# Optimization experiments

Hardware: AMD Instinct MI355X
Metric: run time of the kernel (lower is better)

The kernel has to match this reference:

```python
import jax, jax.numpy as jnp
import numpy as np

D = 128           # embed_dim
NUM_LAYERS = 2
N_CLASSES = 4
OUT_CELL = 64
SPEAKERS = 2
INPUT_DIMS = [768, 74, 35]
B, T = 32, 60


def setup_inputs() -> dict:
    key = jax.random.key(0)
    ks = jax.random.split(key, 24)
    inp = {}
    inp['x0'] = jax.random.normal(ks[0], (B, T, INPUT_DIMS[0]), jnp.float32)
    inp['x1'] = jax.random.normal(ks[1], (B, T, INPUT_DIMS[1]), jnp.float32)
    inp['x2'] = jax.random.normal(ks[2], (B, T, INPUT_DIMS[2]), jnp.float32)
    inp['smask'] = jax.random.normal(ks[3], (B, T, SPEAKERS), jnp.float32)  # argmax -> speaker ids
    # modality projections
    for i, d in enumerate(INPUT_DIMS):
        inp[f'Wp{i}'] = jax.random.normal(ks[4 + i], (d, D), jnp.float32) / np.float32(np.sqrt(d))
        inp[f'bp{i}'] = jnp.zeros((D,), jnp.float32)
    # shared PositionEmbedding (ModuleList([m]*3) shares params)
    inp['freq_emb'] = jax.random.normal(ks[7], (SPEAKERS, D), jnp.float32) * 0.1
    inp['phase_emb'] = jax.random.normal(ks[8], (SPEAKERS, D), jnp.float32)
    # shared QRNNCell (ModuleList([cell]*num_layers) shares params)
    inp['U_x'] = jnp.linalg.qr(jax.random.normal(ks[9], (D, D), jnp.float32))[0]
    inp['U_h'] = jnp.linalg.qr(jax.random.normal(ks[10], (D, D), jnp.float32))[0]
    inp['Lambda'] = jnp.float32(0.5)
    # QMeasurement kernel (real/imag parts of D measurement vectors)
    inp['kernel_r'] = jnp.eye(D, dtype=jnp.float32) + 0.05 * jax.random.normal(ks[11], (D, D), jnp.float32)
    inp['kernel_i'] = 0.05 * jax.random.normal(ks[12], (D, D), jnp.float32)
    # SimpleNet fc_out
    inp['W1'] = jax.random.normal(ks[13], (D, OUT_CELL), jnp.float32) / np.float32(np.sqrt(D))
    inp['b1'] = jnp.zeros((OUT_CELL,), jnp.float32)
    inp['W2'] = jax.random.normal(ks[14], (OUT_CELL, N_CLASSES), jnp.float32) / np.float32(np.sqrt(OUT_CELL))
    inp['b2'] = jnp.zeros((N_CLASSES,), jnp.float32)
    return inp


def _qmn_forward(x0, x1, x2, smask, Wp0, bp0, Wp1, bp1, Wp2, bp2,
                 freq_emb, phase_emb, U_x, U_h, Lambda,
                 kernel_r, kernel_i, W1, b1, W2, b2):
    xs = [x0, x1, x2]
    Ws = [(Wp0, bp0), (Wp1, bp1), (Wp2, bp2)]
    reps = [jax.nn.relu(x @ W + b) for x, (W, b) in zip(xs, Ws)]           # [B,T,D] each
    # mixture weights: softmax over per-modality L2 norms
    norms = jnp.concatenate([jnp.linalg.norm(r, axis=-1, keepdims=True) for r in reps], axis=-1)
    weights = jax.nn.softmax(norms, axis=-1)                               # [B,T,M]
    # shared phase embedding: phase = t * freq[speaker] + phase[speaker]
    ids = jnp.argmax(smask, axis=-1)                                       # [B,T] int
    pos = jnp.arange(T, dtype=jnp.float32)[None, :, None]                  # [1,T,1]
    phase = pos * freq_emb[ids] + phase_emb[ids]                           # [B,T,D]
    cosp, sinp = jnp.cos(phase), jnp.sin(phase)
    # mixed density matrices rho = sum_m w_m |v_m><v_m|
    rho_r = jnp.zeros((B, T, D, D), jnp.float32)
    rho_i = jnp.zeros((B, T, D, D), jnp.float32)
    for m, r in enumerate(reps):
        a = r / jnp.maximum(jnp.linalg.norm(r, axis=-1, keepdims=True), 1e-12)
        pr = a * cosp                                                       # real amplitude
        pi = a * sinp                                                       # imag amplitude
        w = weights[..., m][..., None, None]
        rho_r = rho_r + w * (jnp.einsum('btm,btn->btmn', pr, pr) + jnp.einsum('btm,btn->btmn', pi, pi))
        rho_i = rho_i + w * (jnp.einsum('btm,btn->btmn', pi, pr) - jnp.einsum('btm,btn->btmn', pr, pi))
    # time-major for scan
    sr = jnp.transpose(rho_r, (1, 0, 2, 3))                                # [T,B,D,D]
    si = jnp.transpose(rho_i, (1, 0, 2, 3))

    def cell(h, x):
        hr, hi = h
        xr, xi = x
        Xr = jnp.einsum('mp,bpq,nq->bmn', U_x, xr, U_x)
        Xi = jnp.einsum('mp,bpq,nq->bmn', U_x, xi, U_x)
        Hr = jnp.einsum('mp,bpq,nq->bmn', U_h, hr, U_h)
        Hi = jnp.einsum('mp,bpq,nq->bmn', U_h, hi, U_h)
        nr = Lambda * Hr + (1.0 - Lambda) * Xr
        ni = Lambda * Hi + (1.0 - Lambda) * Xi
        return (nr, ni), (nr, ni)

    h0 = (jnp.broadcast_to(jnp.eye(D, dtype=jnp.float32) / D, (B, D, D)),
          jnp.zeros((B, D, D), jnp.float32))
    for _ in range(NUM_LAYERS):  # same shared cell params each layer
        _, (sr, si) = jax.lax.scan(cell, h0, (sr, si))
    # QMeasurement: p_k = Re(v_k^dag rho v_k), unit-norm complex measurement vectors
    nrm = jnp.sqrt(jnp.sum(kernel_r**2 + kernel_i**2, axis=1, keepdims=True))
    vr = kernel_r / jnp.maximum(nrm, 1e-12)                                # [K,D], K=D
    vi = kernel_i / jnp.maximum(nrm, 1e-12)
    probs = (jnp.einsum('tbmn,km,kn->tbk', sr, vr, vr)
             + jnp.einsum('tbmn,km,kn->tbk', sr, vi, vi)
             - jnp.einsum('tbmn,km,kn->tbk', si, vr, vi)
             + jnp.einsum('tbmn,km,kn->tbk', si, vi, vr))                  # [T,B,D]
    # SimpleNet (dropout = identity at inference)
    hid = jax.nn.relu(probs @ W1 + b1)
    out = jnp.tanh(hid @ W2 + b2)                                          # [T,B,C]
    out = jnp.transpose(out, (1, 0, 2))                                    # [B,T,C]
    return jax.nn.log_softmax(out, axis=2)


def reference(x0, x1, x2, smask, Wp0, bp0, Wp1, bp1, Wp2, bp2,
              freq_emb, phase_emb, U_x, U_h, Lambda,
              kernel_r, kernel_i, W1, b1, W2, b2):
    return _qmn_forward(x0, x1, x2, smask, Wp0, bp0, Wp1, bp1, Wp2, bp2,
                        freq_emb, phase_emb, U_x, U_h, Lambda,
                        kernel_r, kernel_i, W1, b1, W2, b2)
```

## Files before the change

### kernel.cpp

```cpp
#include <hip/hip_runtime.h>


#define DB 32
#define DT 60
#define DD 128
#define BT (DB*DT)
#define SP 136

typedef unsigned short ushort_t;
typedef __attribute__((ext_vector_type(8))) __bf16 bf16x8;
typedef __attribute__((ext_vector_type(8))) unsigned short ushort8_t;
typedef __attribute__((ext_vector_type(4))) float  float4v;

__device__ __forceinline__ float bf2f(ushort_t u){
  union { unsigned int i; float f; } x; x.i = ((unsigned int)u) << 16; return x.f;
}
__device__ __forceinline__ ushort_t f2bf(float f){
  union { float f; unsigned int i; } x; x.f = f;
  unsigned int lsb = (x.i >> 16) & 1u;
  return (ushort_t)((x.i + 0x7FFFu + lsb) >> 16);
}
__device__ __forceinline__ unsigned int f2bfpk(float a, float b){
#if defined(__gfx950__) && __has_builtin(__builtin_amdgcn_cvt_pk_bf16_f32)
  auto v = __builtin_amdgcn_cvt_pk_bf16_f32(a, b);
  unsigned int r; __builtin_memcpy(&r, &v, 4); return r;
#else
  return (unsigned int)f2bf(a) | ((unsigned int)f2bf(b) << 16);
#endif
}
__device__ __forceinline__ void split2(float v, ushort_t& h, ushort_t& l){
  h = f2bf(v); l = f2bf(v - bf2f(h));
}

template<int RT, int CT, bool ALO, bool BLO>
__device__ __forceinline__ void gemm_t(const ushort_t* Ah, const ushort_t* Al,
                                       const ushort_t* Bh, const ushort_t* Bl,
                                       float4v* acc, int row0, int col0, int gma, int q)
{
  for (int ks = 0; ks < 4; ks++){
    int ko = ks*32 + q*8;
    bf16x8 aF[RT], aL[RT], bF[CT], bL[CT];
    #pragma unroll
    for (int R = 0; R < RT; R++){
      int row = row0 + 16*R + gma;
      aF[R] = *(const bf16x8*)&Ah[row*SP + ko];
      if (ALO) aL[R] = *(const bf16x8*)&Al[row*SP + ko];
    }
    #pragma unroll
    for (int C = 0; C < CT; C++){
      int row = col0 + 16*C + gma;
      bF[C] = *(const bf16x8*)&Bh[row*SP + ko];
      if (BLO) bL[C] = *(const bf16x8*)&Bl[row*SP + ko];
    }
    #pragma unroll
    for (int R = 0; R < RT; R++)
      #pragma unroll
      for (int C = 0; C < CT; C++){
        float4v c = acc[R*CT+C];
        c = __builtin_amdgcn_mfma_f32_16x16x32_bf16(aF[R], bF[C], c, 0, 0, 0);
        if (BLO) c = __builtin_amdgcn_mfma_f32_16x16x32_bf16(aF[R], bL[C], c, 0, 0, 0);
        if (ALO) c = __builtin_amdgcn_mfma_f32_16x16x32_bf16(aL[R], bF[C], c, 0, 0, 0);
        acc[R*CT+C] = c;
      }
  }
}

template<int RT, int CT>
__device__ __forceinline__ void emit_t(const float4v* acc, ushort_t* dst, int stride,
                                       int row0, int col0, int gma, int q){
  #pragma unroll
  for (int R = 0; R < RT; R++)
    #pragma unroll
    for (int C = 0; C < CT; C++){
      int c = col0 + 16*C + gma, r0 = row0 + 16*R + 4*q;
      uint2 o;
      o.x = f2bfpk(acc[R*CT+C][0], acc[R*CT+C][1]);
      o.y = f2bfpk(acc[R*CT+C][2], acc[R*CT+C][3]);
      *(uint2*)&dst[(size_t)c*stride + r0] = o;
    }
}
template<int RT, int CT>
__device__ __forceinline__ void emit_split_t(const float4v* acc, ushort_t* dh, ushort_t* dl, int stride,
                                             int row0, int col0, int gma, int q){
  #pragma unroll
  for (int R = 0; R < RT; R++)
    #pragma unroll
    for (int C = 0; C < CT; C++){
      int c = col0 + 16*C + gma, r0 = row0 + 16*R + 4*q;
      ushort4 hh, ll;
      split2(acc[R*CT+C][0], hh.x, ll.x); split2(acc[R*CT+C][1], hh.y, ll.y);
      split2(acc[R*CT+C][2], hh.z, ll.z); split2(acc[R*CT+C][3], hh.w, ll.w);
      *(ushort4*)&dh[(size_t)c*stride + r0] = hh;
      *(ushort4*)&dl[(size_t)c*stride + r0] = ll;
    }
}
template<int NT>
__device__ __forceinline__ void lds_load_mat(ushort_t* dst, const ushort_t* src, int tid){
  for (int i = tid*8; i < 16384; i += NT*8){
    int r = i >> 7, k = i & 127;
    *(ushort8_t*)&dst[r*SP + k] = *(const ushort8_t*)&src[i];
  }
}
template<int NT>
__device__ __forceinline__ void lds_load_rows16(ushort_t* dst, const ushort_t* src, int tid){
  for (int i = tid*8; i < 2048; i += NT*8){
    int r = i >> 7, k = i & 127;
    *(ushort8_t*)&dst[r*SP + k] = *(const ushort8_t*)&src[i];
  }
}
template<int NT>
__device__ __forceinline__ void lds_load_mat2(ushort_t* d0, const ushort_t* s0,
                                              ushort_t* d1, const ushort_t* s1, int tid){
  constexpr int CH = 16384/(NT*8);
  ushort8_t r0[CH], r1[CH];
  #pragma unroll
  for (int c = 0; c < CH; c++) r0[c] = *(const ushort8_t*)&s0[tid*8 + c*NT*8];
  #pragma unroll
  for (int c = 0; c < CH; c++) r1[c] = *(const ushort8_t*)&s1[tid*8 + c*NT*8];
  #pragma unroll
  for (int c = 0; c < CH; c++){
    int i = tid*8 + c*NT*8; int r = i >> 7, k = i & 127;
    *(ushort8_t*)&d0[r*SP + k] = r0[c];
  }
  #pragma unroll
  for (int c = 0; c < CH; c++){
    int i = tid*8 + c*NT*8; int r = i >> 7, k = i & 127;
    *(ushort8_t*)&d1[r*SP + k] = r1[c];
  }
}
template<int NT>
__device__ __forceinline__ void lds_store_mat(ushort_t* dst, const ushort_t* src, int tid){
  for (int i = tid*8; i < 16384; i += NT*8){
    int r = i >> 7, k = i & 127;
    *(ushort8_t*)&dst[i] = *(const ushort8_t*)&src[r*SP + k];
  }
}

__global__ void k_small(const float* Ux, const float* Uh, const float* kr, const float* ki,
                        const float* Wp0, const float* Wp1, const float* Wp2,
                        ushort_t* UxTh, ushort_t* UxTl, ushort_t* UxH, ushort_t* UxL,
                        float* Vr, float* Vi,
                        ushort_t* PpH, ushort_t* PpL, ushort_t* PTh, ushort_t* PTl,
                        ushort_t* WT0h, ushort_t* WT0l, ushort_t* WT1h, ushort_t* WT1l,
                        ushort_t* WT2h, ushort_t* WT2l){
  int blk = blockIdx.x, d = threadIdx.x;
  if (blk < 128){
    int i = blk;
    float v = Ux[i*DD + d];
    ushort_t h, l; split2(v, h, l);
    UxTh[d*DD + i] = h; UxTl[d*DD + i] = l;
  } else if (blk < 256){
    __shared__ float red[DD];
    int k = blk - 128;
    float r = kr[k*DD+d], im = ki[k*DD+d];
    red[d] = r*r + im*im;
    __syncthreads();
    for (int s = 64; s > 0; s >>= 1){ if (d < s) red[d] += red[d+s]; __syncthreads(); }
    float nrm = fmaxf(sqrtf(red[0]), 1e-12f);
    Vr[k*DD+d] = r/nrm; Vi[k*DD+d] = im/nrm;
  } else if (blk < 384){
    int i = blk - 256;
    float v = Uh[i*DD + d];
    ushort_t h, l; split2(v, h, l);
    PpH[i*DD + d] = h;  PpL[i*DD + d] = l;
    PTh[d*DD + i] = h;  PTl[d*DD + i] = l;
  } else {
    int dd2 = blk - 384;
    ushort_t h, l;
    for (int k = d; k < 768; k += 128){
      split2(Wp0[(size_t)k*DD + dd2], h, l);
      WT0h[(size_t)dd2*768 + k] = h; WT0l[(size_t)dd2*768 + k] = l;
    }
    { float v = (d < 74) ? Wp1[(size_t)d*DD + dd2] : 0.f;
      split2(v, h, l); WT1h[dd2*128 + d] = h; WT1l[dd2*128 + d] = l; }
    { float v = (d < 35) ? Wp2[(size_t)d*DD + dd2] : 0.f;
      split2(v, h, l); WT2h[dd2*128 + d] = h; WT2l[dd2*128 + d] = l; }
    { split2(Ux[(size_t)dd2*DD + d], h, l);
      UxH[dd2*DD + d] = h; UxL[dd2*DD + d] = l; }
  }
}

__global__ __launch_bounds__(128) void k_xconv(const float* x0, const float* x1, const float* x2,
    ushort_t* X0h, ushort_t* X0l, ushort_t* X1h, ushort_t* X1l, ushort_t* X2h, ushort_t* X2l){
  int bt = blockIdx.x, d = threadIdx.x;
  ushort_t h, l;
  const float* r0 = x0 + (size_t)bt*768;
  #pragma unroll
  for (int j = 0; j < 6; j++){
    split2(r0[j*128 + d], h, l);
    X0h[(size_t)bt*768 + j*128 + d] = h;
    X0l[(size_t)bt*768 + j*128 + d] = l;
  }
  float v1 = (d < 74) ? x1[(size_t)bt*74 + d] : 0.f;
  split2(v1, h, l);
  X1h[(size_t)bt*128 + d] = h; X1l[(size_t)bt*128 + d] = l;
  float v2 = (d < 35) ? x2[(size_t)bt*35 + d] : 0.f;
  split2(v2, h, l);
  X2h[(size_t)bt*128 + d] = h; X2l[(size_t)bt*128 + d] = l;
}

__global__ __launch_bounds__(512,1) void k_proj(
    const ushort_t* X0h, const ushort_t* X0l, const ushort_t* X1h, const ushort_t* X1l,
    const ushort_t* X2h, const ushort_t* X2l,
    const ushort_t* WT0h, const ushort_t* WT0l, const ushort_t* WT1h, const ushort_t* WT1l,
    const ushort_t* WT2h, const ushort_t* WT2l,
    const float* bp1, const float* bp2,
    float* Rpart, float* Reps)
{
  __shared__ ushort_t Ah[128*SP], Al[128*SP], Bh[128*SP], Bl[128*SP];
  int blk = blockIdx.x;
  int m, tile, ch;
  if (blk < 90){ m = 0; tile = blk/6; ch = blk%6; }
  else if (blk < 105){ m = 1; tile = blk-90; ch = 0; }
  else { m = 2; tile = blk-105; ch = 0; }
  int bt0 = tile*128;
  int tid = threadIdx.x;
  int w = tid >> 6, lane = tid & 63, gma = lane & 15, q = lane >> 4;
  int row0 = 32*(w >> 1), col0 = 64*(w & 1);
  const ushort_t* Wh_ = (m==0)? WT0h : (m==1)? WT1h : WT2h;
  const ushort_t* Wl_ = (m==0)? WT0l : (m==1)? WT1l : WT2l;
  const ushort_t* Xh_ = (m==0)? X0h : (m==1)? X1h : X2h;
  const ushort_t* Xl_ = (m==0)? X0l : (m==1)? X1l : X2l;
  int KX = (m==0)? 768 : 128;
  for (int i = tid*8; i < 16384; i += 4096){
    int r = i >> 7, k = i & 127;
    *(ushort8_t*)&Ah[r*SP + k] = *(const ushort8_t*)&Wh_[(size_t)r*KX + ch*128 + k];
    *(ushort8_t*)&Al[r*SP + k] = *(const ushort8_t*)&Wl_[(size_t)r*KX + ch*128 + k];
    *(ushort8_t*)&Bh[r*SP + k] = *(const ushort8_t*)&Xh_[(size_t)(bt0+r)*KX + ch*128 + k];
    *(ushort8_t*)&Bl[r*SP + k] = *(const ushort8_t*)&Xl_[(size_t)(bt0+r)*KX + ch*128 + k];
  }
  __syncthreads();
  float4v acc[8];
  #pragma unroll
  for (int i = 0; i < 8; i++) acc[i] = (float4v){0.f,0.f,0.f,0.f};
  gemm_t<2,4,true,true>(Ah, Al, Bh, Bl, acc, row0, col0, gma, q);
  if (m == 0){
    #pragma unroll
    for (int R = 0; R < 2; R++)
      #pragma unroll
      for (int C = 0; C < 4; C++){
        int c = col0 + 16*C + gma, r0 = row0 + 16*R + 4*q;
        float4 o;
        o.x = acc[R*4+C][0]; o.y = acc[R*4+C][1];
        o.z = acc[R*4+C][2]; o.w = acc[R*4+C][3];
        *(float4*)&Rpart[((size_t)ch*BT + bt0 + c)*128 + r0] = o;
      }
  } else {
    const float* bp = (m==1)? bp1 : bp2;
    #pragma unroll
    for (int R = 0; R < 2; R++){
      int r0 = row0 + 16*R + 4*q;
      float4 bv = *(const float4*)&bp[r0];
      #pragma unroll
      for (int C = 0; C < 4; C++){
        int c = col0 + 16*C + gma;
        float4v a = acc[R*4+C];
        float4 o;
        o.x = fmaxf(a[0]+bv.x, 0.f); o.y = fmaxf(a[1]+bv.y, 0.f);
        o.z = fmaxf(a[2]+bv.z, 0.f); o.w = fmaxf(a[3]+bv.w, 0.f);
        *(float4*)&Reps[(size_t)(bt0 + c)*384 + m*128 + r0] = o;
      }
    }
  }
}

__global__ __launch_bounds__(128) void k_mix(const float* Rpart, const float* Reps,
    const float* bp0, const float* smask,
    const float* freq, const float* phem, ushort_t* PsH, ushort_t* PsL, float* Wgt)
{
  __shared__ float part[2][3];
  int bt = blockIdx.x; int t = bt % DT;
  int d = threadIdx.x;
  float r0v = bp0[d];
  #pragma unroll
  for (int ch = 0; ch < 6; ch++)
    r0v += Rpart[((size_t)ch*BT + bt)*128 + d];
  r0v = fmaxf(r0v, 0.f);
  float r1v = Reps[(size_t)bt*384 + 128 + d];
  float r2v = Reps[(size_t)bt*384 + 256 + d];
  float s0 = r0v*r0v, s1 = r1v*r1v, s2 = r2v*r2v;
  #pragma unroll
  for (int off = 1; off < 64; off <<= 1){
    s0 += __shfl_xor(s0, off, 64);
    s1 += __shfl_xor(s1, off, 64);
    s2 += __shfl_xor(s2, off, 64);
  }
  int wv = d >> 6;
  if ((d & 63) == 0){ part[wv][0] = s0; part[wv][1] = s1; part[wv][2] = s2; }
  __syncthreads();
  float n0 = sqrtf(part[0][0] + part[1][0]);
  float n1 = sqrtf(part[0][1] + part[1][1]);
  float n2 = sqrtf(part[0][2] + part[1][2]);
  float mx = fmaxf(n0, fmaxf(n1, n2));
  float e0 = expf(n0-mx), e1 = expf(n1-mx), e2 = expf(n2-mx);
  float einv = 1.f/(e0+e1+e2);
  if (d < 3) Wgt[bt*3+d] = (d==0?e0:(d==1?e1:e2))*einv;
  float sm0 = smask[bt*2], sm1 = smask[bt*2+1];
  int id = (sm1 > sm0) ? 1 : 0;
  float ph = (float)t * freq[id*DD+d] + phem[id*DD+d];
  float cp = cosf(ph), sp = sinf(ph);
  float a0 = r0v / fmaxf(n0, 1e-12f);
  float a1 = r1v / fmaxf(n1, 1e-12f);
  float a2 = r2v / fmaxf(n2, 1e-12f);
  ushort_t h, l;
  split2(a0*cp, h, l); PsH[((size_t)0*BT + bt)*DD + d] = h; PsL[((size_t)0*BT + bt)*DD + d] = l;
  split2(a1*cp, h, l); PsH[((size_t)1*BT + bt)*DD + d] = h; PsL[((size_t)1*BT + bt)*DD + d] = l;
  split2(a2*cp, h, l); PsH[((size_t)2*BT + bt)*DD + d] = h; PsL[((size_t)2*BT + bt)*DD + d] = l;
  split2(a0*sp, h, l); PsH[((size_t)3*BT + bt)*DD + d] = h; PsL[((size_t)3*BT + bt)*DD + d] = l;
  split2(a1*sp, h, l); PsH[((size_t)4*BT + bt)*DD + d] = h; PsL[((size_t)4*BT + bt)*DD + d] = l;
  split2(a2*sp, h, l); PsH[((size_t)5*BT + bt)*DD + d] = h; PsL[((size_t)5*BT + bt)*DD + d] = l;
}

__global__ __launch_bounds__(512,1) void k_qtrans(const ushort_t* UxH, const ushort_t* UxL,
                                                  const ushort_t* PsH, const ushort_t* PsL,
                                                  ushort_t* Qb){
  __shared__ ushort_t Ah[128*SP], Al[128*SP], Bh[128*SP], Bl[128*SP];
  int blk = blockIdx.x;
  int tid = threadIdx.x;
  int w = tid >> 6, lane = tid & 63, gma = lane & 15, q = lane >> 4;
  int row0 = 32*(w >> 1), col0 = 64*(w & 1);
  size_t rbase = (size_t)blk*128*128;
  lds_load_mat<512>(Ah, UxH, tid);
  lds_load_mat<512>(Al, UxL, tid);
  lds_load_mat<512>(Bh, PsH + rbase, tid);
  lds_load_mat<512>(Bl, PsL + rbase, tid);
  __syncthreads();
  float4v acc[8];
  #pragma unroll
  for (int i = 0; i < 8; i++) acc[i] = (float4v){0.f,0.f,0.f,0.f};
  gemm_t<2,4,true,true>(Ah, Al, Bh, Bl, acc, row0, col0, gma, q);
  emit_t<2,4>(acc, Qb + rbase, 128, row0, col0, gma, q);
}

__global__ __launch_bounds__(256,2) void k_pow2v2(ushort_t* PpH, ushort_t* PpL,
                                                  ushort_t* PTh, ushort_t* PTl, int s){
  __shared__ ushort_t Ah[128*SP], Al[128*SP], Bh[16*SP], Bl[16*SP];
  int blk = blockIdx.x;
  int which = blk >> 3, sl = blk & 7;
  size_t src = (size_t)(s-1)*16384, dst = (size_t)s*16384;
  int tid = threadIdx.x;
  int w = tid >> 6, lane = tid & 63, gma = lane & 15, q = lane >> 4;
  int row0 = 32*w;
  int gcol0 = sl*16;
  const ushort_t *A_h, *A_l, *B_h, *B_l; ushort_t *D_h, *D_l;
  if (which == 0){ A_h = PTh+src; A_l = PTl+src; B_h = PpH+src; B_l = PpL+src;
                   D_h = PpH+dst; D_l = PpL+dst; }
  else           { A_h = PpH+src; A_l = PpL+src; B_h = PTh+src; B_l = PTl+src;
                   D_h = PTh+dst; D_l = PTl+dst; }
  lds_load_mat<256>(Ah, A_h, tid);
  lds_load_mat<256>(Al, A_l, tid);
  lds_load_rows16<256>(Bh, B_h + (size_t)gcol0*128, tid);
  lds_load_rows16<256>(Bl, B_l + (size_t)gcol0*128, tid);
  __syncthreads();
  float4v acc[2];
  acc[0] = (float4v){0.f,0.f,0.f,0.f};
  acc[1] = (float4v){0.f,0.f,0.f,0.f};
  gemm_t<2,1,true,true>(Ah, Al, Bh, Bl, acc, row0, 0, gma, q);
  emit_split_t<2,1>(acc, D_h, D_l, 128, row0, gcol0, gma, q);
}

__global__ __launch_bounds__(512,1) void k_gchain(const ushort_t* PpH, const ushort_t* PpL,
                                                  const ushort_t* PTh, const ushort_t* PTl,
                                                  ushort_t* GTh, ushort_t* GTl){
  __shared__ ushort_t Ah[128*SP], Al[128*SP], Bh[128*SP], Bl[128*SP];
  int t = blockIdx.x;
  int tid = threadIdx.x;
  int w = tid >> 6, lane = tid & 63, gma = lane & 15, q = lane >> 4;
  int row0 = 32*(w >> 1), col0 = 64*(w & 1);
  size_t gslot = (size_t)t * 16384;
  if (t == 0){
    for (int i = tid*4; i < 16384; i += 2048){
      int r = i >> 7, k = i & 127;
      ushort4 zz; zz.x = zz.y = zz.z = zz.w = 0;
      *(ushort4*)&GTl[gslot + i] = zz;
      ushort4 oh;
      oh.x = (r == (k+0)) ? (ushort_t)0x3F80 : (ushort_t)0;
      oh.y = (r == (k+1)) ? (ushort_t)0x3F80 : (ushort_t)0;
      oh.z = (r == (k+2)) ? (ushort_t)0x3F80 : (ushort_t)0;
      oh.w = (r == (k+3)) ? (ushort_t)0x3F80 : (ushort_t)0;
      *(ushort4*)&GTh[gslot + i] = oh;
    }
    return;
  }
  int b0 = __ffs(t) - 1;
  int rem = t & ~(1 << b0);
  if (rem == 0){
    size_t ps = (size_t)b0 * 16384;
    for (int i = tid*4; i < 16384; i += 2048){
      *(ushort4*)&GTh[gslot + i] = *(const ushort4*)&PTh[ps + i];
      *(ushort4*)&GTl[gslot + i] = *(const ushort4*)&PTl[ps + i];
    }
    return;
  }
  lds_load_mat<512>(Ah, PpH + (size_t)b0*16384, tid);
  lds_load_mat<512>(Al, PpL + (size_t)b0*16384, tid);
  while (rem){
    int k = __ffs(rem) - 1;
    rem &= ~(1 << k);
    lds_load_mat<512>(Bh, PTh + (size_t)k*16384, tid);
    lds_load_mat<512>(Bl, PTl + (size_t)k*16384, tid);
    __syncthreads();
    float4v acc[8];
    #pragma unroll
    for (int i = 0; i < 8; i++) acc[i] = (float4v){0.f,0.f,0.f,0.f};
    if (rem){
      gemm_t<2,4,true,true>(Bh, Bl, Ah, Al, acc, row0, col0, gma, q);
      __syncthreads();
      emit_split_t<2,4>(acc, Ah, Al, SP, row0, col0, gma, q);
      __syncthreads();
    } else {
      gemm_t<2,4,true,true>(Ah, Al, Bh, Bl, acc, row0, col0, gma, q);
      emit_split_t<2,4>(acc, GTh + gslot, GTl + gslot, 128, row0, col0, gma, q);
    }
  }
}

__global__ __launch_bounds__(256,1) void k_precompMW(const ushort_t* GTh, const ushort_t* GTl,
                                                     const ushort_t* UxTh, const ushort_t* UxTl,
                                                     const float* Vr, const float* Vi,
                                                     ushort_t* Mh, ushort_t* Wh){
  __shared__ ushort_t Bh[128*SP], Bl[128*SP], Ah[128*SP], Al[128*SP];
  int blk = blockIdx.x;
  int tid = threadIdx.x;
  int w = tid >> 6, lane = tid & 63, gma = lane & 15, q = lane >> 4;
  int row0 = 64*(w >> 1), col0 = 64*(w & 1);
  if (blk < 60){
    int t = blk;
    lds_load_mat<256>(Bh, GTh + (size_t)t*16384, tid);
    lds_load_mat<256>(Bl, GTl + (size_t)t*16384, tid);
    lds_load_mat<256>(Ah, UxTh, tid);
    lds_load_mat<256>(Al, UxTl, tid);
    __syncthreads();
    float4v acc[16];
    #pragma unroll
    for (int i = 0; i < 16; i++) acc[i] = (float4v){0.f,0.f,0.f,0.f};
    gemm_t<4,4,true,true>(Ah, Al, Bh, Bl, acc, row0, col0, gma, q);
    __syncthreads();
    emit_split_t<4,4>(acc, Ah, Al, SP, row0, col0, gma, q);
    __syncthreads();
    #pragma unroll
    for (int i = 0; i < 16; i++) acc[i] = (float4v){0.f,0.f,0.f,0.f};
    gemm_t<4,4,true,true>(Bh, Bl, Ah, Al, acc, row0, col0, gma, q);
    #pragma unroll
    for (int R = 0; R < 4; R++)
      #pragma unroll
      for (int C = 0; C < 4; C++){
        int c = col0 + 16*C + gma, r0 = row0 + 16*R + 4*q;
        uint2 o;
        o.x = f2bfpk(acc[R*4+C][0], acc[R*4+C][1]);
        o.y = f2bfpk(acc[R*4+C][2], acc[R*4+C][3]);
        *(uint2*)&Mh[(size_t)t*16384 + c*128 + r0] = o;
      }
  } else {
    int bx = blk - 60;
    int t = bx >> 1, which = bx & 1;
    lds_load_mat<256>(Ah, GTh + (size_t)t*16384, tid);
    lds_load_mat<256>(Al, GTl + (size_t)t*16384, tid);
    const float* V = which ? Vi : Vr;
    for (int i = tid; i < 16384; i += 256){
      int r = i >> 7, k = i & 127;
      ushort_t h, l; split2(V[i], h, l);
      Bh[r*SP + k] = h; Bl[r*SP + k] = l;
    }
    __syncthreads();
    float4v acc[16];
    #pragma unroll
    for (int i = 0; i < 16; i++) acc[i] = (float4v){0.f,0.f,0.f,0.f};
    gemm_t<4,4,true,true>(Ah, Al, Bh, Bl, acc, row0, col0, gma, q);
    #pragma unroll
    for (int R = 0; R < 4; R++)
      #pragma unroll
      for (int C = 0; C < 4; C++){
        int c = col0 + 16*C + gma, r0 = row0 + 16*R + 4*q;
        uint2 o;
        o.x = f2bfpk(acc[R*4+C][0], acc[R*4+C][1]);
        o.y = f2bfpk(acc[R*4+C][2], acc[R*4+C][3]);
        *(uint2*)&Wh[(size_t)bx*16384 + c*128 + r0] = o;
      }
  }
}

__global__ __launch_bounds__(512,1) void k_vtrans(const ushort_t* GTh, const ushort_t* Qb, ushort_t* At){
  __shared__ ushort_t Ah[128*SP];
  __shared__ ushort_t Bs[192*SP];
  int t = blockIdx.x;
  int tid = threadIdx.x;
  int w = tid >> 6, lane = tid & 63, gma = lane & 15, q = lane >> 4;
  int row0 = (w & 3)*32, col0 = (w >> 2)*96;
  lds_load_mat<512>(Ah, GTh + (size_t)t*16384, tid);
  for (int i = tid*8; i < 192*128; i += 4096){
    int m = i >> 7, k = i & 127;
    int j = m >> 5, b = m & 31;
    *(ushort8_t*)&Bs[m*SP + k] =
      *(const ushort8_t*)&Qb[((size_t)(j*BT) + b*DT + t)*DD + k];
  }
  __syncthreads();
  float4v acc[12];
  #pragma unroll
  for (int i = 0; i < 12; i++) acc[i] = (float4v){0.f,0.f,0.f,0.f};
  gemm_t<2,6,false,false>(Ah, Ah, Bs, Bs, acc, row0, col0, gma, q);
  emit_t<2,6>(acc, At + (size_t)t*24576, 128, row0, col0, gma, q);
}

__global__ __launch_bounds__(256) void k_zbuild(ushort_t* S, const ushort_t* At,
                                                const float* Wgt, const float* lamp){
  __shared__ ushort_t As[6*DD];
  __shared__ float wl[3];
  int blk = blockIdx.x;
  int b = blk >> 4, slab = blk & 15;
  int tid = threadIdx.x;
  int r = slab*8 + (tid >> 5);
  int c0 = (tid & 31)*4;
  float lam = lamp[0];
  float z0=0.f, z1=0.f, z2=0.f, z3=0.f;
  size_t off = (size_t)slab*1024 + tid*4;
  for (int t = 0; t < DT; t++){
    __syncthreads();
    if (tid < 192){
      int i = tid*4;
      int jj = i >> 7, n = i & 127;
      *(ushort4*)&As[i] = *(const ushort4*)&At[(size_t)t*24576 + (jj*32 + b)*128 + n];
    }
    if (tid < 3) wl[tid] = Wgt[(b*DT + t)*3 + tid];
    __syncthreads();
    float ar[6];
    #pragma unroll
    for (int jj = 0; jj < 6; jj++) ar[jj] = bf2f(As[jj*128 + r]);
    float cb[6];
    cb[0] = wl[0]*(ar[0]+ar[3]); cb[1] = wl[1]*(ar[1]+ar[4]); cb[2] = wl[2]*(ar[2]+ar[5]);
    cb[3] = wl[0]*(ar[3]-ar[0]); cb[4] = wl[1]*(ar[4]-ar[1]); cb[5] = wl[2]*(ar[5]-ar[2]);
    float y0=0.f, y1=0.f, y2=0.f, y3=0.f;
    #pragma unroll
    for (int jj = 0; jj < 6; jj++){
      ushort4 a4 = *(const ushort4*)&As[jj*128 + c0];
      float w_ = cb[jj];
      y0 += w_*bf2f(a4.x); y1 += w_*bf2f(a4.y);
      y2 += w_*bf2f(a4.z); y3 += w_*bf2f(a4.w);
    }
    z0 = lam*z0 + y0; z1 = lam*z1 + y1;
    z2 = lam*z2 + y2; z3 = lam*z3 + y3;
    uint2 o; o.x = f2bfpk(z0, z1); o.y = f2bfpk(z2, z3);
    *(uint2*)&S[((size_t)(t*32 + b))*16384 + off] = o;
  }
}

__global__ __launch_bounds__(512,4) void k_conjmid(ushort_t* S, const ushort_t* Mh,
                                                   const float* lamp){
  __shared__ ushort_t Bh[128*SP], Zs[128*SP];
  int blk = blockIdx.x;
  int t = blk >> 5;
  size_t slot = (size_t)blk * 16384;
  int tid = threadIdx.x;
  int w = tid >> 6, lane = tid & 63, gma = lane & 15, q = lane >> 4;
  int row0 = 32*(w >> 1), col0 = 64*(w & 1);
  lds_load_mat2<512>(Zs, S + slot, Bh, Mh + (size_t)t*16384, tid);
  __syncthreads();
  float lam = lamp[0];
  float oml = 1.f - lam;
  float ct = powf(lam, (float)(t+1)) / 128.f;
  float4v acc[8];
  #pragma unroll
  for (int i = 0; i < 8; i++) acc[i] = (float4v){0.f,0.f,0.f,0.f};
  gemm_t<2,4,false,false>(Zs, Zs, Bh, Bh, acc, row0, col0, gma, q);
  __syncthreads();
  emit_t<2,4>(acc, Zs, SP, row0, col0, gma, q);
  __syncthreads();
  #pragma unroll
  for (int i = 0; i < 8; i++) acc[i] = (float4v){0.f,0.f,0.f,0.f};
  gemm_t<2,4,false,false>(Zs, Zs, Bh, Bh, acc, row0, col0, gma, q);
  __syncthreads();
  #pragma unroll
  for (int R = 0; R < 2; R++)
    #pragma unroll
    for (int C = 0; C < 4; C++){
      int c = col0 + 16*C + gma, r0 = row0 + 16*R + 4*q;
      float v0 = oml*acc[R*4+C][0] + ((c == r0+0) ? ct : 0.f);
      float v1 = oml*acc[R*4+C][1] + ((c == r0+1) ? ct : 0.f);
      float v2 = oml*acc[R*4+C][2] + ((c == r0+2) ? ct : 0.f);
      float v3 = oml*acc[R*4+C][3] + ((c == r0+3) ? ct : 0.f);
      uint2 o; o.x = f2bfpk(v0, v1); o.y = f2bfpk(v2, v3);
      *(uint2*)&Zs[(size_t)c*SP + r0] = o;
    }
  __syncthreads();
  lds_store_mat<512>(S + slot, Zs, tid);
}

__device__ __forceinline__ void prefix_phase(ushort8_t& buf, bool doload,
                                             const ushort_t* Snext, ushort_t* Scur,
                                             float* a, float lam){
  ushort8_t u = buf;
  if (doload) buf = *(const ushort8_t*)Snext;
  #pragma unroll
  for (int i = 0; i < 8; i++) a[i] = lam*a[i] + bf2f(u[i]);
  uint4 o;
  o.x = f2bfpk(a[0],a[1]); o.y = f2bfpk(a[2],a[3]);
  o.z = f2bfpk(a[4],a[5]); o.w = f2bfpk(a[6],a[7]);
  *(uint4*)Scur = o;
}
__global__ __launch_bounds__(128) void k_prefix(ushort_t* S, const float* lamp){
  int blk = blockIdx.x;
  int chain = blk >> 4, slab = blk & 15;
  int tid = threadIdx.x;
  size_t off = (size_t)slab*1024 + tid*8;
  float lam = lamp[0];
  float a[8];
  #pragma unroll
  for (int i = 0; i < 8; i++) a[i] = 0.f;
  size_t addr = (size_t)chain*16384 + off;
  const size_t step = (size_t)32*16384;
  ushort8_t b0 = *(const ushort8_t*)&S[addr];
  ushort8_t b1 = *(const ushort8_t*)&S[addr + step];
  ushort8_t b2 = *(const ushort8_t*)&S[addr + 2*step];
  ushort8_t b3 = *(const ushort8_t*)&S[addr + 3*step];
  for (int t = 0; t < DT; t += 4){
    prefix_phase(b0, t+4 < DT, &S[addr + 4*step], &S[addr], a, lam); addr += step;
    prefix_phase(b1, t+5 < DT, &S[addr + 4*step], &S[addr], a, lam); addr += step;
    prefix_phase(b2, t+6 < DT, &S[addr + 4*step], &S[addr], a, lam); addr += step;
    prefix_phase(b3, t+7 < DT, &S[addr + 4*step], &S[addr], a, lam); addr += step;
  }
}

__global__ __launch_bounds__(512,2) void k_meas(const ushort_t* S, const ushort_t* Wh,
                                                const float* lamp, float* Probs){
  __shared__ ushort_t Vs[128*SP], Cs[128*SP];
  __shared__ float Pd[64];
  int raw = blockIdx.x;
  int tb = (raw & 7) | ((raw >> 4) << 3);
  int h  = (raw >> 3) & 1;
  int t = tb >> 5;
  int tid = threadIdx.x;
  int w = tid >> 6, lane = tid & 63, gma = lane & 15, q = lane >> 4;
  int row0 = 16*(w >> 1);
  int col0 = 64*(w & 1);
  size_t slot = (size_t)tb * 16384;
  size_t wbase = (size_t)(t*2) * 16384;
  ushort8_t creg[4], vreg[4];
  #pragma unroll
  for (int c = 0; c < 4; c++)
    creg[c] = *(const ushort8_t*)&S[slot + tid*8 + c*4096];
  #pragma unroll
  for (int c = 0; c < 4; c++){
    int i = tid*8 + c*4096;
    int r = i >> 7, k = i & 127;
    size_t gsrc = wbase + ((r < 64) ? 0 : 16384) + (size_t)(64*h + (r & 63))*128 + k;
    vreg[c] = *(const ushort8_t*)&Wh[gsrc];
  }
  if (tid < 64) Pd[tid] = 0.f;
  #pragma unroll
  for (int c = 0; c < 4; c++){
    int i = tid*8 + c*4096;
    int r = i >> 7, k = i & 127;
    *(ushort8_t*)&Cs[r*SP + k] = creg[c];
  }
  #pragma unroll
  for (int c = 0; c < 4; c++){
    int i = tid*8 + c*4096;
    int r = i >> 7, k = i & 127;
    *(ushort8_t*)&Vs[r*SP + k] = vreg[c];
  }
  __syncthreads();
  float4v acc[8];
  #pragma unroll
  for (int i = 0; i < 8; i++) acc[i] = (float4v){0.f,0.f,0.f,0.f};
  #pragma unroll
  for (int ks = 0; ks < 4; ks++){
    int ko = ks*32 + q*8;
    bf16x8 aF0 = *(const bf16x8*)&Vs[(row0 + gma)*SP + ko];
    bf16x8 aF1 = *(const bf16x8*)&Vs[(row0 + 64 + gma)*SP + ko];
    bf16x8 bF[4];
    #pragma unroll
    for (int C = 0; C < 4; C++)
      bF[C] = *(const bf16x8*)&Cs[(col0 + 16*C + gma)*SP + ko];
    #pragma unroll
    for (int C = 0; C < 4; C++){
      acc[C]   = __builtin_amdgcn_mfma_f32_16x16x32_bf16(aF0, bF[C], acc[C],   0, 0, 0);
      acc[4+C] = __builtin_amdgcn_mfma_f32_16x16x32_bf16(aF1, bF[C], acc[4+C], 0, 0, 0);
    }
  }
  #pragma unroll
  for (int j = 0; j < 4; j++){
    int kr = row0 + 4*q + j;
    float s = 0.f;
    #pragma unroll
    for (int C = 0; C < 4; C++){
      int m = col0 + 16*C + gma;
      float w0 = bf2f(Vs[kr*SP + m]);
      float w1 = bf2f(Vs[(kr + 64)*SP + m]);
      s += acc[C][j]*(w0 + w1) + acc[4+C][j]*(w1 - w0);
    }
    #pragma unroll
    for (int off = 1; off < 16; off <<= 1)
      s += __shfl_xor(s, off, 64);
    if (gma == 0) atomicAdd(&Pd[kr], s);
  }
  __syncthreads();
  if (tid < 64){
    float lam = lamp[0];
    float ct = powf(lam, (float)(t+1)) / 128.f;
    Probs[(size_t)tb*DD + 64*h + tid] = (1.f - lam)*Pd[tid] + ct;
  }
}

__global__ __launch_bounds__(64) void k_head(const float* Probs, const float* W1, const float* b1,
                        const float* W2, const float* b2, float* out)
{
  __shared__ float ps[DD];
  __shared__ float hid[64];
  __shared__ float ov[4];
  int tb = blockIdx.x;
  int tid = threadIdx.x;
  ps[tid] = Probs[(size_t)tb*DD + tid];
  ps[tid+64] = Probs[(size_t)tb*DD + 64 + tid];
  __syncthreads();
  float acc = b1[tid];
  for (int dd = 0; dd < DD; dd++) acc += ps[dd]*W1[dd*64 + tid];
  hid[tid] = fmaxf(acc, 0.f);
  __syncthreads();
  if (tid < 4){
    float o = b2[tid];
    for (int j = 0; j < 64; j++) o += hid[j]*W2[j*4 + tid];
    ov[tid] = tanhf(o);
  }
  __syncthreads();
  if (tid == 0){
    float m = fmaxf(fmaxf(ov[0],ov[1]), fmaxf(ov[2],ov[3]));
    float lse = logf(expf(ov[0]-m)+expf(ov[1]-m)+expf(ov[2]-m)+expf(ov[3]-m));
    int t = tb >> 5, b = tb & 31;
    float* o = out + ((size_t)(b*DT + t))*4;
    o[0] = ov[0]-m-lse; o[1] = ov[1]-m-lse;
    o[2] = ov[2]-m-lse; o[3] = ov[3]-m-lse;
  }
}

extern "C" void kernel_launch(void* const* d_in, const int* in_sizes, int n_in,
                              void* d_out, int out_size, void* d_ws, size_t ws_size,
                              hipStream_t stream)
{
  const float* x0    = (const float*)d_in[0];
  const float* x1    = (const float*)d_in[1];
  const float* x2    = (const float*)d_in[2];
  const float* smask = (const float*)d_in[3];
  const float* Wp0   = (const float*)d_in[4];
  const float* bp0   = (const float*)d_in[5];
  const float* Wp1   = (const float*)d_in[6];
  const float* bp1   = (const float*)d_in[7];
  const float* Wp2   = (const float*)d_in[8];
  const float* bp2   = (const float*)d_in[9];
  const float* freq  = (const float*)d_in[10];
  const float* phem  = (const float*)d_in[11];
  const float* Ux    = (const float*)d_in[12];
  const float* Uh    = (const float*)d_in[13];
  const float* lamp  = (const float*)d_in[14];
  const float* kr    = (const float*)d_in[15];
  const float* ki    = (const float*)d_in[16];
  const float* W1    = (const float*)d_in[17];
  const float* b1    = (const float*)d_in[18];
  const float* W2    = (const float*)d_in[19];
  const float* b2    = (const float*)d_in[20];

  char* ws = (char*)d_ws;
  auto alignup = [](size_t x){ return (x + 255) & ~(size_t)255; };
  size_t off = 0;
  ushort_t* S   = (ushort_t*)(ws + off); off = alignup(off + (size_t)1920*16384*sizeof(ushort_t));
  ushort_t* Qb  = (ushort_t*)(ws + off); off = alignup(off + (size_t)6*BT*DD*sizeof(ushort_t));
  float* Rpart  = (float*)(ws + off);    off = alignup(off + (size_t)6*BT*DD*sizeof(float));
  float* Reps   = (float*)(ws + off);    off = alignup(off + (size_t)BT*384*sizeof(float));
  ushort_t* PsH = (ushort_t*)(ws + off); off = alignup(off + (size_t)6*BT*DD*sizeof(ushort_t));
  ushort_t* PsL = (ushort_t*)(ws + off); off = alignup(off + (size_t)6*BT*DD*sizeof(ushort_t));
  ushort_t* X0h = (ushort_t*)(ws + off); off = alignup(off + (size_t)BT*768*sizeof(ushort_t));
  ushort_t* X0l = (ushort_t*)(ws + off); off = alignup(off + (size_t)BT*768*sizeof(ushort_t));
  ushort_t* X1h = (ushort_t*)(ws + off); off = alignup(off + (size_t)BT*128*sizeof(ushort_t));
  ushort_t* X1l = (ushort_t*)(ws + off); off = alignup(off + (size_t)BT*128*sizeof(ushort_t));
  ushort_t* X2h = (ushort_t*)(ws + off); off = alignup(off + (size_t)BT*128*sizeof(ushort_t));
  ushort_t* X2l = (ushort_t*)(ws + off); off = alignup(off + (size_t)BT*128*sizeof(ushort_t));
  float* Wgt    = (float*)(ws + off);    off = alignup(off + (size_t)BT*3*sizeof(float));
  float* Vr     = (float*)(ws + off);    off = alignup(off + (size_t)DD*DD*sizeof(float));
  float* Vi     = (float*)(ws + off);    off = alignup(off + (size_t)DD*DD*sizeof(float));
  ushort_t* UxTh = (ushort_t*)(ws + off); off = alignup(off + (size_t)DD*DD*sizeof(ushort_t));
  ushort_t* UxTl = (ushort_t*)(ws + off); off = alignup(off + (size_t)DD*DD*sizeof(ushort_t));
  ushort_t* UxH = (ushort_t*)(ws + off); off = alignup(off + (size_t)DD*DD*sizeof(ushort_t));
  ushort_t* UxL = (ushort_t*)(ws + off); off = alignup(off + (size_t)DD*DD*sizeof(ushort_t));
  float* Probs  = (float*)(ws + off);    off = alignup(off + (size_t)BT*DD*sizeof(float));
  ushort_t* PpH = (ushort_t*)(ws + off); off = alignup(off + (size_t)6*16384*sizeof(ushort_t));
  ushort_t* PpL = (ushort_t*)(ws + off); off = alignup(off + (size_t)6*16384*sizeof(ushort_t));
  ushort_t* PTh = (ushort_t*)(ws + off); off = alignup(off + (size_t)6*16384*sizeof(ushort_t));
  ushort_t* PTl = (ushort_t*)(ws + off); off = alignup(off + (size_t)6*16384*sizeof(ushort_t));
  ushort_t* Mh  = (ushort_t*)(ws + off); off = alignup(off + (size_t)60*16384*sizeof(ushort_t));
  ushort_t* Wmh = (ushort_t*)(ws + off); off = alignup(off + (size_t)120*16384*sizeof(ushort_t));
  ushort_t* GTh = (ushort_t*)(ws + off); off = alignup(off + (size_t)60*16384*sizeof(ushort_t));
  ushort_t* GTl = (ushort_t*)(ws + off); off = alignup(off + (size_t)60*16384*sizeof(ushort_t));
  ushort_t* At  = (ushort_t*)(ws + off); off = alignup(off + (size_t)60*24576*sizeof(ushort_t));
  ushort_t* WT0h = (ushort_t*)(ws + off); off = alignup(off + (size_t)128*768*sizeof(ushort_t));
  ushort_t* WT0l = (ushort_t*)(ws + off); off = alignup(off + (size_t)128*768*sizeof(ushort_t));
  ushort_t* WT1h = (ushort_t*)(ws + off); off = alignup(off + (size_t)128*128*sizeof(ushort_t));
  ushort_t* WT1l = (ushort_t*)(ws + off); off = alignup(off + (size_t)128*128*sizeof(ushort_t));
  ushort_t* WT2h = (ushort_t*)(ws + off); off = alignup(off + (size_t)128*128*sizeof(ushort_t));
  ushort_t* WT2l = (ushort_t*)(ws + off); off = alignup(off + (size_t)128*128*sizeof(ushort_t));
  (void)ws_size; (void)in_sizes; (void)n_in; (void)out_size;

  k_small<<<512, 128, 0, stream>>>(Ux, Uh, kr, ki, Wp0, Wp1, Wp2,
                                   UxTh, UxTl, UxH, UxL, Vr, Vi,
                                   PpH, PpL, PTh, PTl,
                                   WT0h, WT0l, WT1h, WT1l, WT2h, WT2l);
  k_xconv<<<BT, 128, 0, stream>>>(x0, x1, x2, X0h, X0l, X1h, X1l, X2h, X2l);
  k_proj<<<120, 512, 0, stream>>>(X0h, X0l, X1h, X1l, X2h, X2l,
                                  WT0h, WT0l, WT1h, WT1l, WT2h, WT2l,
                                  bp1, bp2, Rpart, Reps);
  k_mix<<<BT, 128, 0, stream>>>(Rpart, Reps, bp0, smask, freq, phem, PsH, PsL, Wgt);
  k_qtrans<<<90, 512, 0, stream>>>(UxH, UxL, PsH, PsL, Qb);
  for (int s = 1; s <= 5; s++)
    k_pow2v2<<<16, 256, 0, stream>>>(PpH, PpL, PTh, PTl, s);
  k_gchain<<<60, 512, 0, stream>>>(PpH, PpL, PTh, PTl, GTh, GTl);
  k_precompMW<<<180, 256, 0, stream>>>(GTh, GTl, UxTh, UxTl, Vr, Vi, Mh, Wmh);
  k_vtrans<<<60, 512, 0, stream>>>(GTh, Qb, At);
  k_zbuild<<<512, 256, 0, stream>>>(S, At, Wgt, lamp);
  k_conjmid<<<1920, 512, 0, stream>>>(S, Mh, lamp);
  k_prefix<<<512, 128, 0, stream>>>(S, lamp);
  k_meas<<<3840, 512, 0, stream>>>(S, Wmh, lamp, Probs);
  k_head<<<BT, 64, 0, stream>>>(Probs, W1, b1, W2, b2, (float*)d_out);
}
```

Before: 332.6 us.

## Double-buffer zbuild LDS loads and halve per-thread work across twice the blocks

k_zbuild now keeps two LDS buffers and prefetches the next timestep's At row and weights into registers while the current step computes. This cuts the two barriers per step to one and hides global-load latency along the serial recurrence over T. Each thread now produces two output columns instead of four, and the grid doubles to 1024 blocks to add parallelism and occupancy. In exchange, per-thread stores shrink to 4 bytes and each block repeats the shared At load.

```diff
diff --git a/kernel.cpp b/kernel.cpp
--- a/kernel.cpp
+++ b/kernel.cpp
@@ -504,43 +504,52 @@
 
 __global__ __launch_bounds__(256) void k_zbuild(ushort_t* S, const ushort_t* At,
                                                 const float* Wgt, const float* lamp){
-  __shared__ ushort_t As[6*DD];
-  __shared__ float wl[3];
+  __shared__ ushort_t As[2][6*DD];
+  __shared__ float wl[2][3];
   int blk = blockIdx.x;
-  int b = blk >> 4, slab = blk & 15;
-  int tid = threadIdx.x;
-  int r = slab*8 + (tid >> 5);
-  int c0 = (tid & 31)*4;
+  int b = blk >> 5, sl2 = blk & 31;
+  int tid = threadIdx.x;
+  int r = sl2*4 + (tid >> 6);
+  int c = (tid*2) & 127;
   float lam = lamp[0];
-  float z0=0.f, z1=0.f, z2=0.f, z3=0.f;
-  size_t off = (size_t)slab*1024 + tid*4;
+  float z0 = 0.f, z1 = 0.f;
+  size_t off = (size_t)sl2*512 + tid*2;
+  ushort4 pre;
+  float wpre = 0.f;
+  int jj0 = 0, n0 = 0;
+  if (tid < 192){
+    int i = tid*4;
+    jj0 = i >> 7; n0 = i & 127;
+    pre = *(const ushort4*)&At[(size_t)(jj0*32 + b)*128 + n0];
+  }
+  if (tid < 3) wpre = Wgt[(b*DT)*3 + tid];
   for (int t = 0; t < DT; t++){
+    int cur = t & 1;
+    if (tid < 192) *(ushort4*)&As[cur][tid*4] = pre;
+    if (tid < 3) wl[cur][tid] = wpre;
     __syncthreads();
-    if (tid < 192){
-      int i = tid*4;
-      int jj = i >> 7, n = i & 127;
-      *(ushort4*)&As[i] = *(const ushort4*)&At[(size_t)t*24576 + (jj*32 + b)*128 + n];
-    }
-    if (tid < 3) wl[tid] = Wgt[(b*DT + t)*3 + tid];
-    __syncthreads();
+    if (t+1 < DT){
+      if (tid < 192)
+        pre = *(const ushort4*)&At[(size_t)(t+1)*24576 + (size_t)(jj0*32 + b)*128 + n0];
+      if (tid < 3) wpre = Wgt[(b*DT + t+1)*3 + tid];
+    }
     float ar[6];
     #pragma unroll
-    for (int jj = 0; jj < 6; jj++) ar[jj] = bf2f(As[jj*128 + r]);
+    for (int jj = 0; jj < 6; jj++) ar[jj] = bf2f(As[cur][jj*128 + r]);
+    float w0 = wl[cur][0], w1 = wl[cur][1], w2 = wl[cur][2];
     float cb[6];
-    cb[0] = wl[0]*(ar[0]+ar[3]); cb[1] = wl[1]*(ar[1]+ar[4]); cb[2] = wl[2]*(ar[2]+ar[5]);
-    cb[3] = wl[0]*(ar[3]-ar[0]); cb[4] = wl[1]*(ar[4]-ar[1]); cb[5] = wl[2]*(ar[5]-ar[2]);
-    float y0=0.f, y1=0.f, y2=0.f, y3=0.f;
+    cb[0] = w0*(ar[0]+ar[3]); cb[1] = w1*(ar[1]+ar[4]); cb[2] = w2*(ar[2]+ar[5]);
+    cb[3] = w0*(ar[3]-ar[0]); cb[4] = w1*(ar[4]-ar[1]); cb[5] = w2*(ar[5]-ar[2]);
+    float y0 = 0.f, y1 = 0.f;
     #pragma unroll
     for (int jj = 0; jj < 6; jj++){
-      ushort4 a4 = *(const ushort4*)&As[jj*128 + c0];
+      unsigned int a2 = *(const unsigned int*)&As[cur][jj*128 + c];
       float w_ = cb[jj];
-      y0 += w_*bf2f(a4.x); y1 += w_*bf2f(a4.y);
-      y2 += w_*bf2f(a4.z); y3 += w_*bf2f(a4.w);
+      y0 += w_*bf2f((ushort_t)(a2 & 0xFFFF));
+      y1 += w_*bf2f((ushort_t)(a2 >> 16));
     }
     z0 = lam*z0 + y0; z1 = lam*z1 + y1;
-    z2 = lam*z2 + y2; z3 = lam*z3 + y3;
-    uint2 o; o.x = f2bfpk(z0, z1); o.y = f2bfpk(z2, z3);
-    *(uint2*)&S[((size_t)(t*32 + b))*16384 + off] = o;
+    *(unsigned int*)&S[((size_t)(t*32 + b))*16384 + off] = f2bfpk(z0, z1);
   }
 }
 
@@ -813,7 +822,7 @@
   k_gchain<<<60, 512, 0, stream>>>(PpH, PpL, PTh, PTl, GTh, GTl);
   k_precompMW<<<180, 256, 0, stream>>>(GTh, GTl, UxTh, UxTl, Vr, Vi, Mh, Wmh);
   k_vtrans<<<60, 512, 0, stream>>>(GTh, Qb, At);
-  k_zbuild<<<512, 256, 0, stream>>>(S, At, Wgt, lamp);
+  k_zbuild<<<1024, 256, 0, stream>>>(S, At, Wgt, lamp);
   k_conjmid<<<1920, 512, 0, stream>>>(S, Mh, lamp);
   k_prefix<<<512, 128, 0, stream>>>(S, lamp);
   k_meas<<<3840, 512, 0, stream>>>(S, Wmh, lamp, Probs);
```

Result: faster. 318.3 us (-4.3%).
